# Kernel optimization log

Measured on AMD Instinct MI355X. Metric: run time of the kernel, lower is better.

## Reference

```python
import jax, jax.numpy as jnp
import numpy as np

N_TOKENS = 8192
IN_FEATURES = 4096
OUT_FEATURES = 4096


def setup_inputs() -> dict:
    key = jax.random.key(0)
    kx, kw, ks = jax.random.split(key, 3)
    x = jax.random.normal(kx, (N_TOKENS, IN_FEATURES), dtype=jnp.float32)
    # int8 weight in [-127, 126], per torch.randint(-127, 127, ...)
    weight = jax.random.randint(kw, (OUT_FEATURES, IN_FEATURES), -127, 127, dtype=jnp.int32).astype(jnp.int8)
    weight_scales = jax.random.uniform(ks, (OUT_FEATURES,), dtype=jnp.float32, minval=0.001, maxval=0.01)
    bias = jnp.zeros((1, OUT_FEATURES), dtype=jnp.float32)
    return {"x": x, "weight": weight, "weight_scales": weight_scales, "bias": bias}


def reference(x, weight, weight_scales, bias):
    # --- dynamic per-token activation quantization (min-max / abs-max) ---
    # scale per token so that max |x| maps to 127
    x_absmax = jnp.max(jnp.abs(x), axis=-1, keepdims=True)          # [T, 1]
    x_scale = x_absmax / 127.0                                       # [T, 1]
    q_x = jnp.clip(jnp.round(x / x_scale), -127, 127).astype(jnp.int8)  # [T, K]

    # --- int8 GEMM with int32 accumulation: q_y = q_x @ weight.T ---
    q_y = jax.lax.dot_general(
        q_x, weight,
        dimension_numbers=(((1,), (1,)), ((), ())),
        preferred_element_type=jnp.int32,
    )                                                                # [T, N] int32

    # --- dequantize: per-channel weight scale x per-token activation scale ---
    y = q_y.astype(jnp.float32) * weight_scales[None, :] * x_scale   # [T, N]
    y = y + bias
    return y
```

## Files before the change

kernel.cpp:

```cpp
#include <hip/hip_runtime.h>
#include <cstdint>
#include <cstddef>

#define T_TOKENS 8192
#define K_DIM 4096
#define N_DIM 4096
#define K_TILES 32

#define PACK_BLOCKS (N_DIM * K_DIM / 4 / 256)
#define QUANT_BLOCKS T_TOKENS

using i32x4 = __attribute__((ext_vector_type(4))) int;

__global__ __launch_bounds__(256) void prep(const int* __restrict__ win,
                                            int8_t* __restrict__ wout,
                                            const float* __restrict__ x,
                                            int8_t* __restrict__ qx,
                                            float* __restrict__ xscale) {
    const int bid = blockIdx.x;
    const int tid = threadIdx.x;

    if (bid < PACK_BLOCKS) {
        const int idx = bid * 256 + tid;
        const i32x4 v = reinterpret_cast<const i32x4*>(win)[idx];
        uint32_t pk = (uint32_t)(v.x & 255) | ((uint32_t)(v.y & 255) << 8) |
                      ((uint32_t)(v.z & 255) << 16) | ((uint32_t)(v.w & 255) << 24);
        reinterpret_cast<int*>(wout)[idx] = (int)pk;
        return;
    }

    const int t = bid - PACK_BLOCKS;
    const float4* row = reinterpret_cast<const float4*>(x + (size_t)t * K_DIM);

    float4 v[4];
    float amax = 0.0f;
#pragma unroll
    for (int i = 0; i < 4; ++i) {
        v[i] = row[i * 256 + tid];
        amax = fmaxf(amax, fabsf(v[i].x));
        amax = fmaxf(amax, fabsf(v[i].y));
        amax = fmaxf(amax, fabsf(v[i].z));
        amax = fmaxf(amax, fabsf(v[i].w));
    }
#pragma unroll
    for (int off = 32; off > 0; off >>= 1)
        amax = fmaxf(amax, __shfl_xor(amax, off));

    __shared__ float red[4];
    if ((tid & 63) == 0) red[tid >> 6] = amax;
    __syncthreads();
    amax = fmaxf(fmaxf(red[0], red[1]), fmaxf(red[2], red[3]));

    const float scale = fmaxf(amax, 1e-30f) * (1.0f / 127.0f);
    if (tid == 0) xscale[t] = scale;

    const float inv = 1.0f / scale;
    int* qrow = reinterpret_cast<int*>(qx + (size_t)t * K_DIM);
#pragma unroll
    for (int i = 0; i < 4; ++i) {
        int q0 = (int)fminf(fmaxf(rintf(v[i].x * inv), -127.0f), 127.0f);
        int q1 = (int)fminf(fmaxf(rintf(v[i].y * inv), -127.0f), 127.0f);
        int q2 = (int)fminf(fmaxf(rintf(v[i].z * inv), -127.0f), 127.0f);
        int q3 = (int)fminf(fmaxf(rintf(v[i].w * inv), -127.0f), 127.0f);
        uint32_t pk = (uint32_t)(q0 & 255) | ((uint32_t)(q1 & 255) << 8) |
                      ((uint32_t)(q2 & 255) << 16) | ((uint32_t)(q3 & 255) << 24);
        qrow[i * 256 + tid] = (int)pk;
    }
}

__global__ __launch_bounds__(512, 2) void int8_gemm(const int8_t* __restrict__ qx,
                                                    const int8_t* __restrict__ w,
                                                    const float* __restrict__ xscale,
                                                    const float* __restrict__ wscale,
                                                    const float* __restrict__ bias,
                                                    float* __restrict__ out) {
    extern __shared__ int8_t lds[];

    const int tid = threadIdx.x;
    const int lane = tid & 63;
    const int wave = tid >> 6;
    const int wr = wave >> 2;
    const int wn = wave & 3;
    const int l16 = lane & 15;
    const int quad = lane >> 4;

    const int wg = ((blockIdx.x & 7) << 6) | ((int)blockIdx.x >> 3);
    const int tm = wg >> 4;
    const int tn = wg & 15;

    const int8_t* gA = qx + (size_t)tm * 256 * K_DIM;
    const int8_t* gB = w + (size_t)tn * 256 * K_DIM;

    const int s_row = tid >> 2;
    const int scol = (((tid & 3) ^ ((s_row >> 1) & 3)) << 4);
    const int fcol = ((quad ^ ((l16 >> 1) & 3)) << 4);

    const int ldsA_rd = (wr * 128 + l16) * 64 + fcol;
    const int ldsB_rd = 32768 + (wn * 64 + l16) * 64 + fcol;

#define STAGE2(buf, op, ksl, k0)                                                        \
    {                                                                                   \
        const int8_t* g_ = ((op) ? gB : gA) +                                           \
                           ((size_t)s_row * K_DIM + (size_t)((k0) + (ksl) * 64 + scol));\
        int8_t* l_ = lds + (buf) * 65536 + (op) * 32768 + (ksl) * 16384 + tid * 16;     \
        __builtin_amdgcn_global_load_lds(                                               \
            (const __attribute__((address_space(1))) void*)g_,                          \
            (__attribute__((address_space(3))) void*)l_, 16, 0, 0);                     \
        __builtin_amdgcn_global_load_lds(                                               \
            (const __attribute__((address_space(1))) void*)(g_ + (size_t)128 * K_DIM),  \
            (__attribute__((address_space(3))) void*)(l_ + 8192), 16, 0, 0);            \
    }

    i32x4 acc[8][4] = {};
    i32x4 af[4], bf[4];

#define READ_B(buf, ksl)                                                     \
    {                                                                        \
        const int8_t* sB_ = lds + (buf) * 65536 + (ksl) * 16384 + ldsB_rd;   \
        _Pragma("unroll") for (int nj = 0; nj < 4; ++nj)                     \
            bf[nj] = *(const i32x4*)(sB_ + nj * 1024);                       \
    }
#define READ_A(buf, ksl, mh)                                                 \
    {                                                                        \
        const int8_t* sA_ =                                                  \
            lds + (buf) * 65536 + (ksl) * 16384 + (mh) * 4096 + ldsA_rd;     \
        _Pragma("unroll") for (int q = 0; q < 4; ++q)                        \
            af[q] = *(const i32x4*)(sA_ + q * 1024);                         \
    }
#define MFMA16(mh)                                                           \
    __builtin_amdgcn_s_setprio(1);                                           \
    _Pragma("unroll") for (int q = 0; q < 4; ++q) {                          \
        _Pragma("unroll") for (int nj = 0; nj < 4; ++nj)                     \
            acc[(mh) * 4 + q][nj] = __builtin_amdgcn_mfma_i32_16x16x64_i8(   \
                af[q], bf[nj], acc[(mh) * 4 + q][nj], 0, 0, 0);              \
    }                                                                        \
    __builtin_amdgcn_s_setprio(0);

    STAGE2(0, 0, 0, 0)
    STAGE2(0, 1, 0, 0)
    STAGE2(0, 0, 1, 0)
    STAGE2(0, 1, 1, 0)

    for (int t = 0; t < K_TILES - 1; ++t) {
        const int cur = t & 1;
        const int nxt = cur ^ 1;
        const int k1 = (t + 1) << 7;

        STAGE2(nxt, 0, 0, k1)
        asm volatile("s_waitcnt vmcnt(6)" ::: "memory");
        __builtin_amdgcn_s_barrier();
        READ_B(cur, 0)
        READ_A(cur, 0, 0)
        MFMA16(0)
        __builtin_amdgcn_s_barrier();

        STAGE2(nxt, 1, 0, k1)
        READ_A(cur, 0, 1)
        MFMA16(1)
        __builtin_amdgcn_s_barrier();

        STAGE2(nxt, 0, 1, k1)
        asm volatile("s_waitcnt vmcnt(6)" ::: "memory");
        __builtin_amdgcn_s_barrier();
        READ_B(cur, 1)
        READ_A(cur, 1, 0)
        MFMA16(0)
        __builtin_amdgcn_s_barrier();

        STAGE2(nxt, 1, 1, k1)
        READ_A(cur, 1, 1)
        MFMA16(1)
        __builtin_amdgcn_s_barrier();
    }

    {
        asm volatile("s_waitcnt vmcnt(4)" ::: "memory");
        __builtin_amdgcn_s_barrier();
        READ_B(1, 0)
        READ_A(1, 0, 0)
        MFMA16(0)
        __builtin_amdgcn_s_barrier();
        READ_A(1, 0, 1)
        MFMA16(1)
        __builtin_amdgcn_s_barrier();
        asm volatile("s_waitcnt vmcnt(0)" ::: "memory");
        __builtin_amdgcn_s_barrier();
        READ_B(1, 1)
        READ_A(1, 1, 0)
        MFMA16(0)
        __builtin_amdgcn_s_barrier();
        READ_A(1, 1, 1)
        MFMA16(1)
    }

    const int row_base = tm * 256 + wr * 128 + quad * 4;
    const int col_base = tn * 256 + wn * 64 + l16;
    float wsv[4], bsv[4];
#pragma unroll
    for (int nj = 0; nj < 4; ++nj) {
        wsv[nj] = wscale[col_base + nj * 16];
        bsv[nj] = bias[col_base + nj * 16];
    }
#pragma unroll
    for (int mi = 0; mi < 8; ++mi) {
#pragma unroll
        for (int r = 0; r < 4; ++r) {
            const int trow = row_base + mi * 16 + r;
            const float xs = xscale[trow];
            float* orow = out + (size_t)trow * N_DIM + col_base;
#pragma unroll
            for (int nj = 0; nj < 4; ++nj)
                orow[nj * 16] = (float)acc[mi][nj][r] * (wsv[nj] * xs) + bsv[nj];
        }
    }
#undef STAGE2
#undef READ_B
#undef READ_A
#undef MFMA16
}

extern "C" void kernel_launch(void* const* d_in, const int* in_sizes, int n_in,
                              void* d_out, int out_size, void* d_ws, size_t ws_size,
                              hipStream_t stream) {
    const float* x = (const float*)d_in[0];
    const int* w_i32 = (const int*)d_in[1];
    const float* wscale = (const float*)d_in[2];
    const float* bias = (const float*)d_in[3];
    float* out = (float*)d_out;

    int8_t* qx = (int8_t*)d_ws;
    float* xscale = (float*)((char*)d_ws + (size_t)T_TOKENS * K_DIM);
    int8_t* wpk = (int8_t*)((char*)d_ws + (size_t)T_TOKENS * K_DIM + 65536);

    static bool attr_set = false;
    if (!attr_set) {
        (void)hipFuncSetAttribute(reinterpret_cast<const void*>(&int8_gemm),
                                  hipFuncAttributeMaxDynamicSharedMemorySize, 131072);
        attr_set = true;
    }

    prep<<<PACK_BLOCKS + QUANT_BLOCKS, 256, 0, stream>>>(w_i32, wpk, x, qx, xscale);

    int8_gemm<<<dim3(512), dim3(512), 131072, stream>>>(qx, wpk, xscale, wscale, bias, out);
}
```

Measured before the change: 389.8 us.

## Load weight operand directly from global into registers, bypassing LDS

```diff
diff --git a/kernel.cpp b/kernel.cpp
--- a/kernel.cpp
+++ b/kernel.cpp
@@ -89,20 +89,18 @@
     const int tn = wg & 15;
 
     const int8_t* gA = qx + (size_t)tm * 256 * K_DIM;
-    const int8_t* gB = w + (size_t)tn * 256 * K_DIM;
 
     const int s_row = tid >> 2;
     const int scol = (((tid & 3) ^ ((s_row >> 1) & 3)) << 4);
     const int fcol = ((quad ^ ((l16 >> 1) & 3)) << 4);
-
     const int ldsA_rd = (wr * 128 + l16) * 64 + fcol;
-    const int ldsB_rd = 32768 + (wn * 64 + l16) * 64 + fcol;
-
-#define STAGE2(buf, op, ksl, k0)                                                        \
+
+    const int8_t* pB = w + (size_t)(tn * 256 + wn * 64 + l16) * K_DIM + quad * 16;
+
+#define STAGE_A(buf, ksl, k0)                                                           \
     {                                                                                   \
-        const int8_t* g_ = ((op) ? gB : gA) +                                           \
-                           ((size_t)s_row * K_DIM + (size_t)((k0) + (ksl) * 64 + scol));\
-        int8_t* l_ = lds + (buf) * 65536 + (op) * 32768 + (ksl) * 16384 + tid * 16;     \
+        const int8_t* g_ = gA + ((size_t)s_row * K_DIM + (size_t)((k0) + (ksl) * 64 + scol)); \
+        int8_t* l_ = lds + (buf) * 32768 + (ksl) * 16384 + tid * 16;                    \
         __builtin_amdgcn_global_load_lds(                                               \
             (const __attribute__((address_space(1))) void*)g_,                          \
             (__attribute__((address_space(3))) void*)l_, 16, 0, 0);                     \
@@ -112,85 +110,80 @@
     }
 
     i32x4 acc[8][4] = {};
-    i32x4 af[4], bf[4];
-
-#define READ_B(buf, ksl)                                                     \
-    {                                                                        \
-        const int8_t* sB_ = lds + (buf) * 65536 + (ksl) * 16384 + ldsB_rd;   \
-        _Pragma("unroll") for (int nj = 0; nj < 4; ++nj)                     \
-            bf[nj] = *(const i32x4*)(sB_ + nj * 1024);                       \
-    }
-#define READ_A(buf, ksl, mh)                                                 \
-    {                                                                        \
-        const int8_t* sA_ =                                                  \
-            lds + (buf) * 65536 + (ksl) * 16384 + (mh) * 4096 + ldsA_rd;     \
-        _Pragma("unroll") for (int q = 0; q < 4; ++q)                        \
-            af[q] = *(const i32x4*)(sA_ + q * 1024);                         \
-    }
-#define MFMA16(mh)                                                           \
-    __builtin_amdgcn_s_setprio(1);                                           \
-    _Pragma("unroll") for (int q = 0; q < 4; ++q) {                          \
-        _Pragma("unroll") for (int nj = 0; nj < 4; ++nj)                     \
-            acc[(mh) * 4 + q][nj] = __builtin_amdgcn_mfma_i32_16x16x64_i8(   \
-                af[q], bf[nj], acc[(mh) * 4 + q][nj], 0, 0, 0);              \
-    }                                                                        \
+    i32x4 af[4];
+    i32x4 bfX[4], bfY[4];
+
+#define BLOAD(SET, ksl, k0)                                                   \
+    _Pragma("unroll") for (int nj = 0; nj < 4; ++nj)                          \
+        SET[nj] = *(const i32x4*)(pB + (size_t)nj * (16 * K_DIM) +            \
+                                  (size_t)((k0) + (ksl) * 64));
+
+#define READ_A(buf, ksl, mh)                                                  \
+    {                                                                         \
+        const int8_t* sA_ =                                                   \
+            lds + (buf) * 32768 + (ksl) * 16384 + (mh) * 4096 + ldsA_rd;      \
+        _Pragma("unroll") for (int q = 0; q < 4; ++q)                         \
+            af[q] = *(const i32x4*)(sA_ + q * 1024);                          \
+    }
+#define MFMA16(mh, SET)                                                       \
+    __builtin_amdgcn_s_setprio(1);                                            \
+    _Pragma("unroll") for (int q = 0; q < 4; ++q) {                           \
+        _Pragma("unroll") for (int nj = 0; nj < 4; ++nj)                      \
+            acc[(mh) * 4 + q][nj] = __builtin_amdgcn_mfma_i32_16x16x64_i8(    \
+                af[q], SET[nj], acc[(mh) * 4 + q][nj], 0, 0, 0);              \
+    }                                                                         \
     __builtin_amdgcn_s_setprio(0);
 
-    STAGE2(0, 0, 0, 0)
-    STAGE2(0, 1, 0, 0)
-    STAGE2(0, 0, 1, 0)
-    STAGE2(0, 1, 1, 0)
+    STAGE_A(0, 0, 0)
+    STAGE_A(0, 1, 0)
+    BLOAD(bfX, 0, 0)
 
     for (int t = 0; t < K_TILES - 1; ++t) {
         const int cur = t & 1;
         const int nxt = cur ^ 1;
+        const int k0t = t << 7;
         const int k1 = (t + 1) << 7;
 
-        STAGE2(nxt, 0, 0, k1)
+        STAGE_A(nxt, 0, k1)
+        BLOAD(bfY, 1, k0t)
         asm volatile("s_waitcnt vmcnt(6)" ::: "memory");
         __builtin_amdgcn_s_barrier();
-        READ_B(cur, 0)
         READ_A(cur, 0, 0)
-        MFMA16(0)
-        __builtin_amdgcn_s_barrier();
-
-        STAGE2(nxt, 1, 0, k1)
+        MFMA16(0, bfX)
+        __builtin_amdgcn_s_barrier();
         READ_A(cur, 0, 1)
-        MFMA16(1)
-        __builtin_amdgcn_s_barrier();
-
-        STAGE2(nxt, 0, 1, k1)
+        MFMA16(1, bfX)
+        __builtin_amdgcn_s_barrier();
+
+        STAGE_A(nxt, 1, k1)
+        BLOAD(bfX, 0, k1)
         asm volatile("s_waitcnt vmcnt(6)" ::: "memory");
         __builtin_amdgcn_s_barrier();
-        READ_B(cur, 1)
         READ_A(cur, 1, 0)
-        MFMA16(0)
-        __builtin_amdgcn_s_barrier();
-
-        STAGE2(nxt, 1, 1, k1)
+        MFMA16(0, bfY)
+        __builtin_amdgcn_s_barrier();
         READ_A(cur, 1, 1)
-        MFMA16(1)
+        MFMA16(1, bfY)
         __builtin_amdgcn_s_barrier();
     }
 
     {
+        BLOAD(bfY, 1, (K_TILES - 1) << 7)
         asm volatile("s_waitcnt vmcnt(4)" ::: "memory");
         __builtin_amdgcn_s_barrier();
-        READ_B(1, 0)
         READ_A(1, 0, 0)
-        MFMA16(0)
+        MFMA16(0, bfX)
         __builtin_amdgcn_s_barrier();
         READ_A(1, 0, 1)
-        MFMA16(1)
+        MFMA16(1, bfX)
         __builtin_amdgcn_s_barrier();
         asm volatile("s_waitcnt vmcnt(0)" ::: "memory");
         __builtin_amdgcn_s_barrier();
-        READ_B(1, 1)
         READ_A(1, 1, 0)
-        MFMA16(0)
+        MFMA16(0, bfY)
         __builtin_amdgcn_s_barrier();
         READ_A(1, 1, 1)
-        MFMA16(1)
+        MFMA16(1, bfY)
     }
 
     const int row_base = tm * 256 + wr * 128 + quad * 4;
@@ -213,8 +206,8 @@
                 orow[nj * 16] = (float)acc[mi][nj][r] * (wsv[nj] * xs) + bsv[nj];
         }
     }
-#undef STAGE2
-#undef READ_B
+#undef STAGE_A
+#undef BLOAD
 #undef READ_A
 #undef MFMA16
 }
@@ -235,11 +228,11 @@
     static bool attr_set = false;
     if (!attr_set) {
         (void)hipFuncSetAttribute(reinterpret_cast<const void*>(&int8_gemm),
-                                  hipFuncAttributeMaxDynamicSharedMemorySize, 131072);
+                                  hipFuncAttributeMaxDynamicSharedMemorySize, 65536);
         attr_set = true;
     }
 
     prep<<<PACK_BLOCKS + QUANT_BLOCKS, 256, 0, stream>>>(w_i32, wpk, x, qx, xscale);
 
-    int8_gemm<<<dim3(512), dim3(512), 131072, stream>>>(qx, wpk, xscale, wscale, bias, out);
+    int8_gemm<<<dim3(512), dim3(512), 65536, stream>>>(qx, wpk, xscale, wscale, bias, out);
 }
```

After: 473.3 us. 21.4% more time.
